# Performance work log

Hardware: AMD Instinct MI355X
Metric: run time of the kernel (lower is better)

## Reference

```python
import jax, jax.numpy as jnp
import numpy as np

B, S, E, H = 4, 2048, 1024, 16
D = E // H  # head_dim


def setup_inputs() -> dict:
    key = jax.random.key(0)
    ks = jax.random.split(key, 5)
    scale = 1.0 / np.sqrt(E)
    return {
        "qkv": jax.random.normal(ks[0], (B, S, E), jnp.float32),
        "in_w": jax.random.normal(ks[1], (3 * E, E), jnp.float32) * scale,
        "in_b": jax.random.normal(ks[2], (3 * E,), jnp.float32) * scale,
        "out_w": jax.random.normal(ks[3], (E, E), jnp.float32) * scale,
        "out_b": jax.random.normal(ks[4], (E,), jnp.float32) * scale,
    }


def reference(qkv, in_w, in_b, out_w, out_b):
    # in_proj: torch Linear -> x @ W^T + b, output [B,S,3E]
    x1 = jnp.einsum('bse,fe->bsf', qkv, in_w) + in_b
    q, k, v = jnp.split(x1, 3, axis=2)  # each [B,S,E]
    # reshape to heads: [B,H,S,D] (contiguous head_dim slices == reshape)
    q = q.reshape(B, S, H, D).transpose(0, 2, 1, 3)
    k = k.reshape(B, S, H, D).transpose(0, 2, 1, 3)
    v = v.reshape(B, S, H, D).transpose(0, 2, 1, 3)
    scores = jnp.einsum('bhqd,bhkd->bhqk', q, k) / jnp.sqrt(jnp.float32(D))
    attn = jax.nn.softmax(scores, axis=-1)  # dropout p=0.0 -> identity
    out = jnp.einsum('bhqk,bhkd->bhqd', attn, v)  # [B,H,S,D]
    out = out.transpose(0, 2, 1, 3).reshape(B, S, E)
    return jnp.einsum('bse,fe->bsf', out, out_w) + out_b
```

## Files before the change

kernel.cpp:

```cpp
#include <hip/hip_runtime.h>


typedef __attribute__((ext_vector_type(8))) short s16x8;
typedef __attribute__((ext_vector_type(8))) __bf16 bf16x8;
typedef __attribute__((ext_vector_type(4))) float f32x4;
typedef __attribute__((ext_vector_type(16))) float f32x16;
typedef __attribute__((ext_vector_type(4))) unsigned short u16x4;
typedef __attribute__((ext_vector_type(4))) unsigned int u32x4;

#define QSCALE_F 0.18033688011112042f

#if __has_builtin(__builtin_amdgcn_exp2f)
#define EXP2F(x) __builtin_amdgcn_exp2f(x)
#else
#define EXP2F(x) exp2f(x)
#endif

__device__ __forceinline__ unsigned short f2bf(float f) {
  unsigned int u = __builtin_bit_cast(unsigned int, f);
  u += 0x7fffu + ((u >> 16) & 1u);
  return (unsigned short)(u >> 16);
}

__device__ __forceinline__ f32x4 mfma16(s16x8 a, s16x8 b, f32x4 c) {
  return __builtin_amdgcn_mfma_f32_16x16x32_bf16(
      __builtin_bit_cast(bf16x8, a), __builtin_bit_cast(bf16x8, b), c, 0, 0, 0);
}
__device__ __forceinline__ f32x16 mfma32(s16x8 a, s16x8 b, f32x16 c) {
  return __builtin_amdgcn_mfma_f32_32x32x16_bf16(
      __builtin_bit_cast(bf16x8, a), __builtin_bit_cast(bf16x8, b), c, 0, 0, 0);
}

__device__ __forceinline__ unsigned cvtpk(float lo, float hi) {
  unsigned r;
  asm("v_cvt_pk_bf16_f32 %0, %1, %2" : "=v"(r) : "v"(lo), "v"(hi));
  return r;
}
__device__ __forceinline__ void p32swap(unsigned &a, unsigned &b) {
  asm volatile("v_permlane32_swap_b32 %0, %1" : "+v"(a), "+v"(b));
}

#define GLL16(gp, lp) __builtin_amdgcn_global_load_lds(                       \
    (const __attribute__((address_space(1))) void*)(gp),                      \
    (__attribute__((address_space(3))) void*)(lp), 16, 0, 0)

#define SBAR0 __builtin_amdgcn_sched_barrier(0)
#define HWBAR __builtin_amdgcn_s_barrier()
#define LGKM0 asm volatile("s_waitcnt lgkmcnt(0)" ::: "memory")
#define VMC5 asm volatile("s_waitcnt vmcnt(5)" ::: "memory")
#define VMC2 asm volatile("s_waitcnt vmcnt(2)" ::: "memory")
#define VMC1 asm volatile("s_waitcnt vmcnt(1)" ::: "memory")
#define VMC0 asm volatile("s_waitcnt vmcnt(0)" ::: "memory")
#define PRIO1 __builtin_amdgcn_s_setprio(1)
#define PRIO0 __builtin_amdgcn_s_setprio(0)

__global__ void cvt_all(const float* __restrict__ qkv,
                        const float* __restrict__ in_w,
                        const float* __restrict__ out_w,
                        unsigned short* __restrict__ qkv_bf,
                        unsigned short* __restrict__ win_bf,
                        unsigned short* __restrict__ wout_bf) {
  int i = (blockIdx.x * 256 + threadIdx.x) * 4;
  const int stride = gridDim.x * 256 * 4;
  for (; i < 12582912; i += stride) {
    const float* src;
    unsigned short* dst;
    int off;
    float sc = 1.0f;
    if (i < 8388608) {
      src = qkv; dst = qkv_bf; off = i;
    } else if (i < 11534336) {
      off = i - 8388608; src = in_w; dst = win_bf;
      if (off < 1048576) sc = QSCALE_F;
    } else {
      off = i - 11534336; src = out_w; dst = wout_bf;
    }
    const float4 v = *reinterpret_cast<const float4*>(src + off);
    u16x4 r;
    r.x = f2bf(v.x * sc); r.y = f2bf(v.y * sc);
    r.z = f2bf(v.z * sc); r.w = f2bf(v.w * sc);
    *reinterpret_cast<u16x4*>(dst + off) = r;
  }
}

__global__ __launch_bounds__(512, 2) void gemm1_8ph(
    const unsigned short* __restrict__ A, const unsigned short* __restrict__ B,
    const float* __restrict__ bias, unsigned short* __restrict__ C,
    int M, int N, int K, int qscale_cols) {
  __shared__ __align__(16) unsigned short As[2][256 * 64];
  __shared__ __align__(16) unsigned short Bs[2][192 * 64];
  const int NT = K >> 6;
  const int id = blockIdx.x;
  const int xc = id & 7, r0 = id >> 3;
  const int mi_ = xc * 4 + (r0 & 3);
  const int ni_ = r0 >> 2;
  const int bm = mi_ * 256, bn = ni_ * 192;

  const int tid = threadIdx.x;
  const int lane = tid & 63, w = tid >> 6;
  const int l15 = lane & 15, l4 = (lane >> 4) & 3;
  const int wm = w >> 2, wn = w & 3;
  const int swz = (l15 & 7) << 4;

#define STG_U(ldsc_, gb_, unit_, ktel_) {                                     \
    const int o = (unit_) * 8192 + tid * 16;                                  \
    const int row_ = o >> 7;                                                  \
    const int cb_ = (o & 127) ^ ((row_ & 7) << 4);                            \
    GLL16((gb_) + (size_t)row_ * K + (ktel_) + (cb_ >> 1),                    \
          (char*)(ldsc_) + o);                                                \
  }
#define RD_A(buf_, qm_, dst_) {                                               \
    _Pragma("unroll") for (int mt = 0; mt < 4; ++mt)                          \
      _Pragma("unroll") for (int kk = 0; kk < 2; ++kk)                        \
        dst_[mt][kk] = *(const s16x8*)((const char*)As[buf_] +                \
            (wm * 128 + (qm_) * 64 + mt * 16 + l15) * 128 +                   \
            ((kk * 64 + l4 * 16) ^ swz));                                     \
  }
#define RD_B01(buf_, dst_) {                                                  \
    _Pragma("unroll") for (int nt = 0; nt < 2; ++nt)                          \
      _Pragma("unroll") for (int kk = 0; kk < 2; ++kk)                        \
        dst_[nt][kk] = *(const s16x8*)((const char*)Bs[buf_] +                \
            (wn * 48 + nt * 16 + l15) * 128 +                                 \
            ((kk * 64 + l4 * 16) ^ swz));                                     \
  }
#define RD_B2(buf_, dst_) {                                                   \
    _Pragma("unroll") for (int kk = 0; kk < 2; ++kk)                          \
      dst_[kk] = *(const s16x8*)((const char*)Bs[buf_] +                      \
          (wn * 48 + 32 + l15) * 128 + ((kk * 64 + l4 * 16) ^ swz));          \
  }
#define MM16(qm_) {                                                           \
    _Pragma("unroll") for (int mt = 0; mt < 4; ++mt)                          \
      _Pragma("unroll") for (int nt = 0; nt < 2; ++nt)                        \
        _Pragma("unroll") for (int kk = 0; kk < 2; ++kk)                      \
          acc[(qm_) * 4 + mt][nt] = mfma16(                                   \
              a[mt][kk], b01[nt][kk], acc[(qm_) * 4 + mt][nt]);               \
  }
#define MM8(qm_) {                                                            \
    _Pragma("unroll") for (int mt = 0; mt < 4; ++mt)                          \
      _Pragma("unroll") for (int kk = 0; kk < 2; ++kk)                        \
        acc[(qm_) * 4 + mt][2] = mfma16(                                      \
            a[mt][kk], b2[kk], acc[(qm_) * 4 + mt][2]);                       \
  }

  f32x4 acc[8][3];
#pragma unroll
  for (int i = 0; i < 8; ++i)
#pragma unroll
    for (int j = 0; j < 3; ++j) acc[i][j] = (f32x4){0.f, 0.f, 0.f, 0.f};

  const unsigned short* Ag = A + (size_t)bm * K;
  const unsigned short* Bg = B + (size_t)bn * K;

  STG_U(Bs[0], Bg, 0, 0); STG_U(Bs[0], Bg, 1, 0); STG_U(Bs[0], Bg, 2, 0);
  STG_U(As[0], Ag, 0, 0); STG_U(As[0], Ag, 2, 0);
  STG_U(As[0], Ag, 1, 0); STG_U(As[0], Ag, 3, 0);
  VMC0;
  SBAR0; HWBAR;

  s16x8 a[4][2], b01[2][2], b2[2];
  for (int t = 0; t < NT; ++t) {
    const int cur = t & 1, oth = cur ^ 1;
    const bool st = (t + 1 < NT);
    const int kel = (t + 1) * 64;
    RD_A(cur, 0, a);
    RD_B01(cur, b01);
    if (st) { STG_U(Bs[oth], Bg, 0, kel); STG_U(Bs[oth], Bg, 1, kel);
              STG_U(Bs[oth], Bg, 2, kel); }
    SBAR0; HWBAR; LGKM0; SBAR0;
    PRIO1; MM16(0); PRIO0;
    SBAR0; HWBAR;
    RD_B2(cur, b2);
    if (st) { STG_U(As[oth], Ag, 0, kel); STG_U(As[oth], Ag, 2, kel); }
    SBAR0; HWBAR; LGKM0; SBAR0;
    PRIO1; MM8(0); PRIO0;
    SBAR0;
    if (st) { VMC5; } else { VMC0; }
    HWBAR;
    RD_A(cur, 1, a);
    if (st) { STG_U(As[oth], Ag, 1, kel); STG_U(As[oth], Ag, 3, kel); }
    SBAR0; HWBAR; LGKM0; SBAR0;
    PRIO1; MM8(1); PRIO0;
    SBAR0; HWBAR;
    PRIO1; MM16(1); PRIO0;
    SBAR0;
    if (st) { VMC2; } else { VMC0; }
    HWBAR;
  }

#pragma unroll
  for (int mi = 0; mi < 8; ++mi)
#pragma unroll
    for (int ni = 0; ni < 3; ++ni) {
      const int col = bn + wn * 48 + ni * 16 + l15;
      const float bsc = (col < qscale_cols) ? QSCALE_F : 1.0f;
      const float bv = bias[col] * bsc;
#pragma unroll
      for (int r = 0; r < 4; ++r) {
        const int row = bm + wm * 128 + mi * 16 + l4 * 4 + r;
        C[(size_t)row * N + col] = f2bf(acc[mi][ni][r] + bv);
      }
    }
#undef STG_U
#undef RD_A
#undef RD_B01
#undef RD_B2
#undef MM16
#undef MM8
}

template <bool OUT_BF16>
__global__ __launch_bounds__(256, 2) void gemm_nt(
    const unsigned short* __restrict__ A, const unsigned short* __restrict__ B,
    const float* __restrict__ bias, void* __restrict__ Cout,
    int M, int N, int K, int qscale_cols) {
  __shared__ __align__(16) unsigned short As[128 * 64];
  __shared__ __align__(16) unsigned short Bs[128 * 64];
  const int tid = threadIdx.x;
  const int lane = tid & 63, w = tid >> 6;
  const int l15 = lane & 15, l4 = lane >> 4;
  const int wr = w >> 1, wc = w & 1;
  const int bm = blockIdx.y * 128, bn = blockIdx.x * 128;

  f32x4 acc[4][4];
#pragma unroll
  for (int i = 0; i < 4; ++i)
#pragma unroll
    for (int j = 0; j < 4; ++j) acc[i][j] = (f32x4){0.f, 0.f, 0.f, 0.f};

  for (int kt = 0; kt < K; kt += 64) {
#pragma unroll
    for (int j = 0; j < 4; ++j) {
      const int gb = (j * 4 + w) * 64;
      const int g = gb + lane;
      const int row = g >> 3, seg = g & 7;
      GLL16(A + (size_t)(bm + row) * K + kt + seg * 8, As + gb * 8);
      GLL16(B + (size_t)(bn + row) * K + kt + seg * 8, Bs + gb * 8);
    }
    __syncthreads();
#pragma unroll
    for (int kk = 0; kk < 2; ++kk) {
      s16x8 a[4], b[4];
#pragma unroll
      for (int mi = 0; mi < 4; ++mi)
        a[mi] = *reinterpret_cast<const s16x8*>(
            As + (wr * 64 + mi * 16 + l15) * 64 + kk * 32 + l4 * 8);
#pragma unroll
      for (int ni = 0; ni < 4; ++ni)
        b[ni] = *reinterpret_cast<const s16x8*>(
            Bs + (wc * 64 + ni * 16 + l15) * 64 + kk * 32 + l4 * 8);
#pragma unroll
      for (int mi = 0; mi < 4; ++mi)
#pragma unroll
        for (int ni = 0; ni < 4; ++ni)
          acc[mi][ni] = mfma16(a[mi], b[ni], acc[mi][ni]);
    }
    __syncthreads();
  }
#pragma unroll
  for (int mi = 0; mi < 4; ++mi) {
#pragma unroll
    for (int ni = 0; ni < 4; ++ni) {
      const int col = bn + wc * 64 + ni * 16 + l15;
      const float bsc = (col < qscale_cols) ? QSCALE_F : 1.0f;
      const float bv = bias[col] * bsc;
#pragma unroll
      for (int r = 0; r < 4; ++r) {
        const int row = bm + wr * 64 + mi * 16 + l4 * 4 + r;
        const float val = acc[mi][ni][r] + bv;
        if (OUT_BF16)
          ((unsigned short*)Cout)[(size_t)row * N + col] = f2bf(val);
        else
          ((float*)Cout)[(size_t)row * N + col] = val;
      }
    }
  }
}

__global__ __launch_bounds__(512, 2) void attn_fwd(
    const unsigned short* __restrict__ X1, unsigned short* __restrict__ O) {
  __shared__ __align__(16) unsigned short Ks[3][64 * 64];
  __shared__ __align__(16) unsigned short Vt[2][64 * 64];

  const int id = blockIdx.x;
  const int xc = id & 7, r0 = id >> 3;
  const int bh = xc * 8 + (r0 & 7);
  const int qt = r0 >> 3;
  const int b = bh >> 4, h = bh & 15;
  const int tid = threadIdx.x;
  const int lane = tid & 63, w = tid >> 6;
  const int l31 = lane & 31, hi = lane >> 5;

  const unsigned short* Qp = X1 + (size_t)b * 2048 * 3072 + h * 64;
  const unsigned short* Kp = Qp + 1024;
  const unsigned short* Vp = Qp + 2048;
  const int q0 = qt * 256 + w * 32;

  s16x8 qf[4];
#pragma unroll
  for (int kk = 0; kk < 4; ++kk)
    qf[kk] = *reinterpret_cast<const s16x8*>(
        Qp + (size_t)(q0 + l31) * 3072 + kk * 16 + hi * 8);

  f32x16 oacc[2];
#pragma unroll
  for (int db = 0; db < 2; ++db)
#pragma unroll
    for (int i = 0; i < 16; ++i) oacc[db][i] = 0.f;
  float l_r = 0.f;

#define STAGE_K(kt_, buf_)                                                    \
  {                                                                           \
    const int chunk = w * 1024;                                               \
    const int o = chunk + lane * 16;                                          \
    const int row = o >> 7;                                                   \
    const int srcb = (o & 127) ^ ((row & 7) << 4);                            \
    GLL16(Kp + (size_t)((kt_) + row) * 3072 + (srcb >> 1),                    \
          (char*)Ks[buf_] + chunk);                                           \
  }
#define LOAD_V(kt_, vr_)                                                      \
  {                                                                           \
    vr_ = *reinterpret_cast<const s16x8*>(                                    \
        Vp + (size_t)((kt_) + lane) * 3072 + w * 8);                          \
  }
#define WRITE_V(vr_, buf_)                                                    \
  {                                                                           \
    _Pragma("unroll") for (int e = 0; e < 8; ++e) {                           \
      const int d = w * 8 + e;                                                \
      const int byt = d * 128 + ((lane * 2) ^ (e << 4));                      \
      *(unsigned short*)((char*)Vt[buf_] + byt) = (unsigned short)vr_[e];     \
    }                                                                         \
  }

  s16x8 vnxt;
  LOAD_V(0, vnxt);
  STAGE_K(0, 0);
  STAGE_K(64, 1);
  SBAR0;
  VMC1;
  WRITE_V(vnxt, 0);
  LGKM0;
  HWBAR;

  for (int t = 0; t < 32; ++t) {
    const unsigned short* Ksc = Ks[t % 3];
    const unsigned short* Vtc = Vt[t & 1];
    if (t < 31) LOAD_V((t + 1) * 64, vnxt);
    if (t < 30) STAGE_K((t + 2) * 64, (t + 2) % 3);
    SBAR0;

    f32x16 sa[2];
#pragma unroll
    for (int sub = 0; sub < 2; ++sub)
#pragma unroll
      for (int i = 0; i < 16; ++i) sa[sub][i] = 0.f;
    PRIO1;
#pragma unroll
    for (int sub = 0; sub < 2; ++sub) {
      const int row = sub * 32 + l31;
#pragma unroll
      for (int kk = 0; kk < 4; ++kk) {
        const int byt = row * 128 + ((kk * 32 + hi * 16) ^ ((l31 & 7) << 4));
        s16x8 ka = *reinterpret_cast<const s16x8*>((const char*)Ksc + byt);
        sa[sub] = mfma32(ka, qf[kk], sa[sub]);
      }
    }
    PRIO0;

    float s0 = 0.f, s1 = 0.f, s2 = 0.f, s3 = 0.f;
#pragma unroll
    for (int sub = 0; sub < 2; ++sub)
#pragma unroll
      for (int i = 0; i < 16; i += 4) {
        sa[sub][i]     = EXP2F(sa[sub][i]);     s0 += sa[sub][i];
        sa[sub][i + 1] = EXP2F(sa[sub][i + 1]); s1 += sa[sub][i + 1];
        sa[sub][i + 2] = EXP2F(sa[sub][i + 2]); s2 += sa[sub][i + 2];
        sa[sub][i + 3] = EXP2F(sa[sub][i + 3]); s3 += sa[sub][i + 3];
      }
    float rsum = (s0 + s1) + (s2 + s3);
    rsum += __shfl_xor(rsum, 32);
    l_r += rsum;

    s16x8 pa[2][2];
#pragma unroll
    for (int sub = 0; sub < 2; ++sub)
#pragma unroll
      for (int g = 0; g < 2; ++g) {
        unsigned c0 = cvtpk(sa[sub][g * 8 + 0], sa[sub][g * 8 + 1]);
        unsigned c1 = cvtpk(sa[sub][g * 8 + 2], sa[sub][g * 8 + 3]);
        unsigned c2 = cvtpk(sa[sub][g * 8 + 4], sa[sub][g * 8 + 5]);
        unsigned c3 = cvtpk(sa[sub][g * 8 + 6], sa[sub][g * 8 + 7]);
        p32swap(c0, c2);
        p32swap(c1, c3);
        u32x4 tt = {c0, c1, c2, c3};
        pa[sub][g] = __builtin_bit_cast(s16x8, tt);
      }

    PRIO1;
#pragma unroll
    for (int db = 0; db < 2; ++db) {
      const int row = db * 32 + l31;
#pragma unroll
      for (int sub = 0; sub < 2; ++sub)
#pragma unroll
        for (int g = 0; g < 2; ++g) {
          const int byt =
              row * 128 + (((sub * 2 + g) * 32 + hi * 16) ^ ((l31 & 7) << 4));
          s16x8 vb = *reinterpret_cast<const s16x8*>((const char*)Vtc + byt);
          oacc[db] = mfma32(pa[sub][g], vb, oacc[db]);
        }
    }
    PRIO0;

    if (t < 31) {
      if (t < 30) { VMC1; } else { VMC0; }
      WRITE_V(vnxt, (t + 1) & 1);
      LGKM0;
      HWBAR;
    }
  }

  const float invl = 1.0f / l_r;
#pragma unroll
  for (int r = 0; r < 16; ++r) {
    const int crow = (r & 3) + 8 * (r >> 2) + 4 * hi;
    const float ir = __shfl(invl, crow);
    const size_t base = (size_t)(b * 2048 + q0 + crow) * 1024 + h * 64 + l31;
    O[base] = f2bf(oacc[0][r] * ir);
    O[base + 32] = f2bf(oacc[1][r] * ir);
  }
}

extern "C" void kernel_launch(void* const* d_in, const int* in_sizes, int n_in,
                              void* d_out, int out_size, void* d_ws,
                              size_t ws_size, hipStream_t stream) {
  const float* qkv   = (const float*)d_in[0];
  const float* in_w  = (const float*)d_in[1];
  const float* in_b  = (const float*)d_in[2];
  const float* out_w = (const float*)d_in[3];
  const float* out_b = (const float*)d_in[4];
  float* out = (float*)d_out;
  char* ws = (char*)d_ws;

  unsigned short* qkv_bf  = (unsigned short*)(ws);
  unsigned short* win_bf  = (unsigned short*)(ws + 16777216);
  unsigned short* wout_bf = (unsigned short*)(ws + 23068672);
  unsigned short* x1      = (unsigned short*)(ws + 25165824);
  unsigned short* attn_out = qkv_bf;

  cvt_all<<<2048, 256, 0, stream>>>(qkv, in_w, out_w, qkv_bf, win_bf, wout_bf);

  gemm1_8ph<<<512, 512, 0, stream>>>(
      qkv_bf, win_bf, in_b, x1, 8192, 3072, 1024, 1024);

  attn_fwd<<<512, 512, 0, stream>>>(x1, attn_out);

  gemm_nt<false><<<dim3(8, 64), 256, 0, stream>>>(
      attn_out, wout_bf, out_b, (void*)out, 8192, 1024, 1024, 0);
}
```

Measured before the change: 180.5 us.

## Replace output-projection GEMM with double-buffered 8-phase 256x128 tile kernel

Replaces the simple single-buffered 128x128 output projection GEMM with a 512-thread kernel. It uses 256x128 tiles, double-buffered LDS with XOR swizzling, and an interleaved phase schedule that overlaps global-to-LDS loads with MFMA work. A grouped block index remap is added for L2 locality. The aim is to hide memory latency and avoid LDS bank conflicts in the last GEMM. In exchange the grid drops to 256 blocks, which may underfill the GPU.

Result: no change. 178.6 us, median of 2 (-1.0%).

```diff
diff --git a/kernel.cpp b/kernel.cpp
--- a/kernel.cpp
+++ b/kernel.cpp
@@ -48,6 +48,7 @@
 #define HWBAR __builtin_amdgcn_s_barrier()
 #define LGKM0 asm volatile("s_waitcnt lgkmcnt(0)" ::: "memory")
 #define VMC5 asm volatile("s_waitcnt vmcnt(5)" ::: "memory")
+#define VMC4 asm volatile("s_waitcnt vmcnt(4)" ::: "memory")
 #define VMC2 asm volatile("s_waitcnt vmcnt(2)" ::: "memory")
 #define VMC1 asm volatile("s_waitcnt vmcnt(1)" ::: "memory")
 #define VMC0 asm volatile("s_waitcnt vmcnt(0)" ::: "memory")
@@ -208,72 +209,111 @@
 #undef MM8
 }
 
-template <bool OUT_BF16>
-__global__ __launch_bounds__(256, 2) void gemm_nt(
+__global__ __launch_bounds__(512, 2) void gemm2_8ph(
     const unsigned short* __restrict__ A, const unsigned short* __restrict__ B,
-    const float* __restrict__ bias, void* __restrict__ Cout,
-    int M, int N, int K, int qscale_cols) {
-  __shared__ __align__(16) unsigned short As[128 * 64];
-  __shared__ __align__(16) unsigned short Bs[128 * 64];
+    const float* __restrict__ bias, float* __restrict__ C,
+    int M, int N, int K) {
+  __shared__ __align__(16) unsigned short As[2][256 * 64];
+  __shared__ __align__(16) unsigned short Bs[2][128 * 64];
+  const int NT = K >> 6;
+  const int id = blockIdx.x;
+  const int mi_ = (id & 7) * 4 + ((id >> 3) & 3);
+  const int ni_ = id >> 5;
+  const int bm = mi_ * 256, bn = ni_ * 128;
+
   const int tid = threadIdx.x;
   const int lane = tid & 63, w = tid >> 6;
-  const int l15 = lane & 15, l4 = lane >> 4;
-  const int wr = w >> 1, wc = w & 1;
-  const int bm = blockIdx.y * 128, bn = blockIdx.x * 128;
-
-  f32x4 acc[4][4];
-#pragma unroll
-  for (int i = 0; i < 4; ++i)
-#pragma unroll
-    for (int j = 0; j < 4; ++j) acc[i][j] = (f32x4){0.f, 0.f, 0.f, 0.f};
-
-  for (int kt = 0; kt < K; kt += 64) {
-#pragma unroll
-    for (int j = 0; j < 4; ++j) {
-      const int gb = (j * 4 + w) * 64;
-      const int g = gb + lane;
-      const int row = g >> 3, seg = g & 7;
-      GLL16(A + (size_t)(bm + row) * K + kt + seg * 8, As + gb * 8);
-      GLL16(B + (size_t)(bn + row) * K + kt + seg * 8, Bs + gb * 8);
-    }
-    __syncthreads();
-#pragma unroll
-    for (int kk = 0; kk < 2; ++kk) {
-      s16x8 a[4], b[4];
-#pragma unroll
-      for (int mi = 0; mi < 4; ++mi)
-        a[mi] = *reinterpret_cast<const s16x8*>(
-            As + (wr * 64 + mi * 16 + l15) * 64 + kk * 32 + l4 * 8);
-#pragma unroll
-      for (int ni = 0; ni < 4; ++ni)
-        b[ni] = *reinterpret_cast<const s16x8*>(
-            Bs + (wc * 64 + ni * 16 + l15) * 64 + kk * 32 + l4 * 8);
-#pragma unroll
-      for (int mi = 0; mi < 4; ++mi)
-#pragma unroll
-        for (int ni = 0; ni < 4; ++ni)
-          acc[mi][ni] = mfma16(a[mi], b[ni], acc[mi][ni]);
-    }
-    __syncthreads();
-  }
-#pragma unroll
-  for (int mi = 0; mi < 4; ++mi) {
-#pragma unroll
-    for (int ni = 0; ni < 4; ++ni) {
-      const int col = bn + wc * 64 + ni * 16 + l15;
-      const float bsc = (col < qscale_cols) ? QSCALE_F : 1.0f;
-      const float bv = bias[col] * bsc;
+  const int l15 = lane & 15, l4 = (lane >> 4) & 3;
+  const int wm = w >> 2, wn = w & 3;
+  const int swz = (l15 & 7) << 4;
+
+#define STG_U(ldsc_, gb_, unit_, ktel_) {                                     \
+    const int o = (unit_) * 8192 + tid * 16;                                  \
+    const int row_ = o >> 7;                                                  \
+    const int cb_ = (o & 127) ^ ((row_ & 7) << 4);                            \
+    GLL16((gb_) + (size_t)row_ * K + (ktel_) + (cb_ >> 1),                    \
+          (char*)(ldsc_) + o);                                                \
+  }
+#define RD_A(buf_, qm_, dst_) {                                               \
+    _Pragma("unroll") for (int mt = 0; mt < 4; ++mt)                          \
+      _Pragma("unroll") for (int kk = 0; kk < 2; ++kk)                        \
+        dst_[mt][kk] = *(const s16x8*)((const char*)As[buf_] +                \
+            (wm * 128 + (qm_) * 64 + mt * 16 + l15) * 128 +                   \
+            ((kk * 64 + l4 * 16) ^ swz));                                     \
+  }
+#define RD_B(buf_, qn_, dst_) {                                               \
+    _Pragma("unroll") for (int kk = 0; kk < 2; ++kk)                          \
+      dst_[kk] = *(const s16x8*)((const char*)Bs[buf_] +                      \
+          (wn * 32 + (qn_) * 16 + l15) * 128 +                                \
+          ((kk * 64 + l4 * 16) ^ swz));                                       \
+  }
+#define MMQ(qm_, qn_, b_) {                                                   \
+    _Pragma("unroll") for (int mt = 0; mt < 4; ++mt)                          \
+      _Pragma("unroll") for (int kk = 0; kk < 2; ++kk)                        \
+        acc[(qm_) * 4 + mt][qn_] = mfma16(                                    \
+            a[mt][kk], b_[kk], acc[(qm_) * 4 + mt][qn_]);                     \
+  }
+
+  f32x4 acc[8][2];
+#pragma unroll
+  for (int i = 0; i < 8; ++i)
+#pragma unroll
+    for (int j = 0; j < 2; ++j) acc[i][j] = (f32x4){0.f, 0.f, 0.f, 0.f};
+
+  const unsigned short* Ag = A + (size_t)bm * K;
+  const unsigned short* Bg = B + (size_t)bn * K;
+
+  STG_U(Bs[0], Bg, 0, 0); STG_U(Bs[0], Bg, 1, 0);
+  STG_U(As[0], Ag, 0, 0); STG_U(As[0], Ag, 2, 0);
+  STG_U(As[0], Ag, 1, 0); STG_U(As[0], Ag, 3, 0);
+  VMC0;
+  SBAR0; HWBAR;
+
+  s16x8 a[4][2], b0[2], b1[2];
+  for (int t = 0; t < NT; ++t) {
+    const int cur = t & 1, oth = cur ^ 1;
+    const bool st = (t + 1 < NT);
+    const int kel = (t + 1) * 64;
+    RD_A(cur, 0, a);
+    RD_B(cur, 0, b0);
+    if (st) { STG_U(Bs[oth], Bg, 0, kel); STG_U(Bs[oth], Bg, 1, kel); }
+    SBAR0; HWBAR; LGKM0; SBAR0;
+    PRIO1; MMQ(0, 0, b0); PRIO0;
+    SBAR0; HWBAR;
+    RD_B(cur, 1, b1);
+    if (st) { STG_U(As[oth], Ag, 0, kel); STG_U(As[oth], Ag, 2, kel); }
+    SBAR0; HWBAR; LGKM0; SBAR0;
+    PRIO1; MMQ(0, 1, b1); PRIO0;
+    SBAR0;
+    if (st) { VMC4; } else { VMC0; }
+    HWBAR;
+    RD_A(cur, 1, a);
+    if (st) { STG_U(As[oth], Ag, 1, kel); STG_U(As[oth], Ag, 3, kel); }
+    SBAR0; HWBAR; LGKM0; SBAR0;
+    PRIO1; MMQ(1, 1, b1); PRIO0;
+    SBAR0; HWBAR;
+    PRIO1; MMQ(1, 0, b0); PRIO0;
+    SBAR0;
+    if (st) { VMC2; } else { VMC0; }
+    HWBAR;
+  }
+
+#pragma unroll
+  for (int mi = 0; mi < 8; ++mi)
+#pragma unroll
+    for (int ni = 0; ni < 2; ++ni) {
+      const int col = bn + wn * 32 + ni * 16 + l15;
+      const float bv = bias[col];
 #pragma unroll
       for (int r = 0; r < 4; ++r) {
-        const int row = bm + wr * 64 + mi * 16 + l4 * 4 + r;
-        const float val = acc[mi][ni][r] + bv;
-        if (OUT_BF16)
-          ((unsigned short*)Cout)[(size_t)row * N + col] = f2bf(val);
-        else
-          ((float*)Cout)[(size_t)row * N + col] = val;
+        const int row = bm + wm * 128 + mi * 16 + l4 * 4 + r;
+        C[(size_t)row * N + col] = acc[mi][ni][r] + bv;
       }
     }
-  }
+#undef STG_U
+#undef RD_A
+#undef RD_B
+#undef MMQ
 }
 
 __global__ __launch_bounds__(512, 2) void attn_fwd(
@@ -454,6 +494,6 @@
 
   attn_fwd<<<512, 512, 0, stream>>>(x1, attn_out);
 
-  gemm_nt<false><<<dim3(8, 64), 256, 0, stream>>>(
-      attn_out, wout_bf, out_b, (void*)out, 8192, 1024, 1024, 0);
-}
+  gemm2_8ph<<<256, 512, 0, stream>>>(
+      attn_out, wout_bf, out_b, out, 8192, 1024, 1024);
+}
```
